# Optimization experiments

Hardware: AMD Instinct MI355X
Metric: run time of the kernel (lower is better)

The kernel has to match this reference:

```python
import jax, jax.numpy as jnp
import numpy as np

N, S, IN_F, TEXT_D, EMB, H = 128, 1024, 768, 512, 512, 8
HD = EMB // H  # 64


def setup_inputs() -> dict:
    key = jax.random.key(0)
    ks = jax.random.split(key, 14)
    sc = 0.02
    return {
        "v": jax.random.normal(ks[0], (1, N, 12, IN_F), dtype=jnp.float32),
        "t": jax.random.normal(ks[1], (N, S, TEXT_D), dtype=jnp.float32),
        "t_len": jax.random.randint(ks[2], (N,), 1, S + 1, dtype=jnp.int32),
        "W_fc1": jax.random.normal(ks[3], (EMB, IN_F), dtype=jnp.float32) * sc,
        "b_fc1": jnp.zeros((EMB,), jnp.float32),
        "W_fc2": jax.random.normal(ks[4], (EMB, 12 * EMB), dtype=jnp.float32) * sc,
        "b_fc2": jnp.zeros((EMB,), jnp.float32),
        "Wq": jax.random.normal(ks[5], (EMB, EMB), dtype=jnp.float32) * sc,
        "Wk": jax.random.normal(ks[6], (EMB, TEXT_D), dtype=jnp.float32) * sc,
        "Wv": jax.random.normal(ks[7], (EMB, TEXT_D), dtype=jnp.float32) * sc,
        "bq": jnp.zeros((EMB,), jnp.float32),
        "bk": jnp.zeros((EMB,), jnp.float32),
        "bv": jnp.zeros((EMB,), jnp.float32),
        "Wo": jax.random.normal(ks[8], (EMB, EMB), dtype=jnp.float32) * sc,
        "bo": jnp.zeros((EMB,), jnp.float32),
    }


def reference(v, t, t_len, W_fc1, b_fc1, W_fc2, b_fc2, Wq, Wk, Wv, bq, bk, bv, Wo, bo):
    # fc1 + ReLU: [1,N,12,IN_F] -> [N,12,EMB]
    x = jax.nn.relu(jnp.einsum('onif,ef->onie', v, W_fc1) + b_fc1)[0]
    # flatten + fc2 + ReLU -> [N, EMB]
    x = x.reshape(N, 12 * EMB)
    vfeat = jax.nn.relu(x @ W_fc2.T + b_fc2)
    # Batched ragged multihead attention, query length 1 per item.
    scale = 1.0 / jnp.sqrt(jnp.asarray(HD, vfeat.dtype))
    q = ((vfeat @ Wq.T + bq) * scale).reshape(N, H, HD)           # [N,H,HD]
    k = (jnp.einsum('nsd,ed->nse', t, Wk) + bk).reshape(N, S, H, HD)
    vv = (jnp.einsum('nsd,ed->nse', t, Wv) + bv).reshape(N, S, H, HD)
    scores = jnp.einsum('nhd,nshd->nhs', q, k)                    # [N,H,S]
    valid = (jnp.arange(S)[None, :] < t_len[:, None])[:, None, :]  # [N,1,S]
    scores = jnp.where(valid, scores, jnp.finfo(scores.dtype).min)
    w = jax.nn.softmax(scores, axis=-1)                           # [N,H,S]
    ctx = jnp.einsum('nhs,nshd->nhd', w, vv).reshape(N, EMB)
    attn_out = ctx @ Wo.T + bo                                    # [N,EMB]
    return vfeat, attn_out
```

## Files before the change

kernel.cpp:

```cpp
#include <hip/hip_runtime.h>

#define NB 128
#define SSEQ 1024
#define TD 512
#define TSTR 516

typedef _Float16 half8 __attribute__((ext_vector_type(8)));
typedef _Float16 half4 __attribute__((ext_vector_type(4)));
typedef float f32x4 __attribute__((ext_vector_type(4)));

template<int AM, int BM>
__device__ __forceinline__ void gemm_body(
    const void* __restrict__ Av, int lda, long aSZ,
    const void* __restrict__ Bv, int ldb, long bSZ,
    const float* __restrict__ bias, const float* __restrict__ aRowScale,
    float scale, int doRelu, int outMode,
    float* __restrict__ outF, _Float16* __restrict__ outH,
    int ldc, int cColOff, int kTiles, long oSplit,
    int mt, int nt, int sp, int bz, int tid)
{
  __shared__ _Float16 As[64][72];
  __shared__ _Float16 Bs[64][72];
  int r = tid >> 2, kq = (tid & 3) * 16;
  int w = tid >> 6, l = tid & 63;
  long aoff = (long)bz * aSZ + (long)(mt * 64 + r) * lda + (long)sp * kTiles * 64 + kq;
  long boff = (long)bz * bSZ + (long)(nt * 64 + r) * ldb + (long)sp * kTiles * 64 + kq;
  const _Float16* apH = (const _Float16*)Av + aoff;
  const float*    apF = (const float*)Av + aoff;
  const _Float16* bpH = (const _Float16*)Bv + boff;
  const float*    bpF = (const float*)Bv + boff;
  float srA = 1.0f;
  if constexpr (AM == 2) srA = 1.0f / aRowScale[(mt * 64 + r) * 8 + sp];

  half8 pa0, pa1, pb0, pb1;
  f32x4 qa0, qa1, qa2, qa3, qc0, qc1, qc2, qc3;
  if constexpr (AM == 0) { pa0 = *(const half8*)apH; pa1 = *(const half8*)(apH + 8); }
  else { qa0 = *(const f32x4*)apF; qa1 = *(const f32x4*)(apF + 4);
         qa2 = *(const f32x4*)(apF + 8); qa3 = *(const f32x4*)(apF + 12); }
  if constexpr (BM == 0) { pb0 = *(const half8*)bpH; pb1 = *(const half8*)(bpH + 8); }
  else { qc0 = *(const f32x4*)bpF; qc1 = *(const f32x4*)(bpF + 4);
         qc2 = *(const f32x4*)(bpF + 8); qc3 = *(const f32x4*)(bpF + 12); }

  f32x4 acc[4];
  #pragma unroll
  for (int c = 0; c < 4; ++c) acc[c] = (f32x4){0.f, 0.f, 0.f, 0.f};
  int fr = l & 15, fo = (l >> 4) * 8;
  for (int kt = 0; kt < kTiles; ++kt) {
    __syncthreads();
    if constexpr (AM == 0) {
      *(half8*)&As[r][kq] = pa0; *(half8*)&As[r][kq + 8] = pa1;
    } else {
      f32x4 s0 = qa0, s1 = qa1, s2 = qa2, s3 = qa3;
      if constexpr (AM == 2) { s0 *= srA; s1 *= srA; s2 *= srA; s3 *= srA; }
      *(half4*)&As[r][kq + 0]  = __builtin_convertvector(s0, half4);
      *(half4*)&As[r][kq + 4]  = __builtin_convertvector(s1, half4);
      *(half4*)&As[r][kq + 8]  = __builtin_convertvector(s2, half4);
      *(half4*)&As[r][kq + 12] = __builtin_convertvector(s3, half4);
    }
    if constexpr (BM == 0) {
      *(half8*)&Bs[r][kq] = pb0; *(half8*)&Bs[r][kq + 8] = pb1;
    } else {
      *(half4*)&Bs[r][kq + 0]  = __builtin_convertvector(qc0, half4);
      *(half4*)&Bs[r][kq + 4]  = __builtin_convertvector(qc1, half4);
      *(half4*)&Bs[r][kq + 8]  = __builtin_convertvector(qc2, half4);
      *(half4*)&Bs[r][kq + 12] = __builtin_convertvector(qc3, half4);
    }
    __syncthreads();
    if (kt + 1 < kTiles) {
      apH += 64; apF += 64; bpH += 64; bpF += 64;
      if constexpr (AM == 0) { pa0 = *(const half8*)apH; pa1 = *(const half8*)(apH + 8); }
      else { qa0 = *(const f32x4*)apF; qa1 = *(const f32x4*)(apF + 4);
             qa2 = *(const f32x4*)(apF + 8); qa3 = *(const f32x4*)(apF + 12); }
      if constexpr (BM == 0) { pb0 = *(const half8*)bpH; pb1 = *(const half8*)(bpH + 8); }
      else { qc0 = *(const f32x4*)bpF; qc1 = *(const f32x4*)(bpF + 4);
             qc2 = *(const f32x4*)(bpF + 8); qc3 = *(const f32x4*)(bpF + 12); }
    }
    #pragma unroll
    for (int ks = 0; ks < 2; ++ks) {
      half8 af = *(const half8*)&As[16 * w + fr][ks * 32 + fo];
      #pragma unroll
      for (int c = 0; c < 4; ++c) {
        half8 bf = *(const half8*)&Bs[16 * c + fr][ks * 32 + fo];
        acc[c] = __builtin_amdgcn_mfma_f32_16x16x32_f16(af, bf, acc[c], 0, 0, 0);
      }
    }
  }
  int lrow = (l >> 4) * 4, lcol = l & 15;
  #pragma unroll
  for (int c = 0; c < 4; ++c) {
    #pragma unroll
    for (int rr = 0; rr < 4; ++rr) {
      int gm = mt * 64 + 16 * w + lrow + rr;
      int gn = nt * 64 + 16 * c + lcol;
      int ecol = gn + bz * cColOff;
      float vv = acc[c][rr];
      if (bias && sp == 0) vv += bias[ecol];
      vv *= scale;
      if (doRelu) vv = fmaxf(vv, 0.f);
      long oidx = (long)gm * ldc + ecol;
      if (outMode == 0) outF[oidx] = vv;
      else if (outMode == 1) outH[oidx] = (_Float16)vv;
      else if (outMode == 2) outF[oidx + (long)sp * oSplit] = vv;
      else atomicAdd(&outF[oidx], vv);
    }
  }
}

template<int AM, int BM>
__global__ __launch_bounds__(256) void k_gemm(
    const void* __restrict__ Av, int lda, long aSZ,
    const void* __restrict__ Bv, int ldb, long bSZ,
    const float* __restrict__ bias, const float* __restrict__ aRowScale,
    float scale, int doRelu, int outMode,
    float* __restrict__ outF, _Float16* __restrict__ outH,
    int ldc, int cColOff, int mtiles, int kTiles, long oSplit)
{
  gemm_body<AM, BM>(Av, lda, aSZ, Bv, ldb, bSZ, bias, aRowScale, scale, doRelu,
                    outMode, outF, outH, ldc, cColOff, kTiles, oSplit,
                    (int)blockIdx.x % mtiles, (int)blockIdx.x / mtiles,
                    (int)blockIdx.y, (int)blockIdx.z, (int)threadIdx.x);
}

__global__ __launch_bounds__(256) void k_prepfc1(
    const float* __restrict__ Wq, const float* __restrict__ Wk,
    const float* __restrict__ bq, const float* __restrict__ bk,
    _Float16* __restrict__ G16T, float* __restrict__ gb,
    float* __restrict__ qbc, float* __restrict__ cvec,
    float* __restrict__ pz, _Float16* __restrict__ qz,
    const float* __restrict__ v, const float* __restrict__ W1,
    const float* __restrict__ b1, _Float16* __restrict__ x16,
    const float* __restrict__ Wv, const float* __restrict__ Wo,
    const float* __restrict__ bv, _Float16* __restrict__ M16,
    float* __restrict__ obo8)
{
  int bx = blockIdx.x, tid = threadIdx.x;
  if (bx >= 1024) {
    int s = bx - 1024;
    gemm_body<1, 1>(v, 768, 0, W1, 768, 0, b1, nullptr, 1.f, 1, 1,
                    nullptr, x16, 512, 0, 12, 0, s % 24, s / 24, 0, 0, tid);
    return;
  }
  __shared__ float SA[64][68];
  __shared__ float SB[64][68];
  __shared__ float sv0[64], sv1[64];
  int r = tid >> 2, cq = (tid & 3) * 16;
  int te = tid & 15, td = tid >> 4;

  if (bx >= 512) {
    int b2 = bx - 512;
    int h = b2 >> 6, et = (b2 >> 3) & 7, gt = b2 & 7;
    const float* wvp = Wv + (long)(h * 64 + r) * 512 + gt * 64 + cq;
    const float* wop = Wo + (long)(et * 64 + r) * 512 + h * 64 + cq;
    #pragma unroll
    for (int c = 0; c < 4; ++c)
      *(f32x4*)&SA[r][cq + 4 * c] = *(const f32x4*)(wvp + 4 * c);
    #pragma unroll
    for (int c = 0; c < 4; ++c) {
      f32x4 x = *(const f32x4*)(wop + 4 * c);
      #pragma unroll
      for (int i = 0; i < 4; ++i) SB[cq + 4 * c + i][r] = x[i];
    }
    if (tid < 64) sv0[tid] = bv[h * 64 + tid];
    __syncthreads();
    float acc[4][4];
    #pragma unroll
    for (int a = 0; a < 4; ++a)
      #pragma unroll
      for (int d = 0; d < 4; ++d) acc[a][d] = 0.f;
    #pragma unroll 4
    for (int jj = 0; jj < 64; ++jj) {
      f32x4 av = *(const f32x4*)&SA[jj][te * 4];
      f32x4 bt = *(const f32x4*)&SB[jj][td * 4];
      #pragma unroll
      for (int a = 0; a < 4; ++a)
        #pragma unroll
        for (int d = 0; d < 4; ++d) acc[a][d] = fmaf(av[a], bt[d], acc[a][d]);
    }
    #pragma unroll
    for (int d = 0; d < 4; ++d) {
      half4 hv = { (_Float16)acc[0][d], (_Float16)acc[1][d],
                   (_Float16)acc[2][d], (_Float16)acc[3][d] };
      *(half4*)(M16 + (long)(et * 64 + td * 4 + d) * 4096 + h * 512 + gt * 64 + te * 4) = hv;
    }
    if (gt == 0 && te == 0) {
      float s0 = 0.f, s1 = 0.f, s2 = 0.f, s3 = 0.f;
      for (int jj = 0; jj < 64; ++jj) {
        f32x4 bt = *(const f32x4*)&SB[jj][td * 4];
        float bb = sv0[jj];
        s0 = fmaf(bt[0], bb, s0); s1 = fmaf(bt[1], bb, s1);
        s2 = fmaf(bt[2], bb, s2); s3 = fmaf(bt[3], bb, s3);
      }
      obo8[h * 512 + et * 64 + td * 4 + 0] = s0;
      obo8[h * 512 + et * 64 + td * 4 + 1] = s1;
      obo8[h * 512 + et * 64 + td * 4 + 2] = s2;
      obo8[h * 512 + et * 64 + td * 4 + 3] = s3;
    }
    return;
  }

  int b = bx;
  int gid = b * 256 + tid;
  for (long i = gid; i < 131328; i += 131072)
    *(f32x4*)(pz + 4 * i) = (f32x4){0.f, 0.f, 0.f, 0.f};
  {
    long i4 = (long)gid * 4;
    long n = i4 >> 12, off = i4 & 4095;
    *(half4*)(qz + n * 8192 + 4096 + off) = (half4){(_Float16)0, (_Float16)0, (_Float16)0, (_Float16)0};
  }
  int h = b >> 6, et = (b >> 3) & 7, dt = b & 7;
  const float* wqp = Wq + (long)(h * 64 + r) * 512 + et * 64 + cq;
  const float* wkp = Wk + (long)(h * 64 + r) * 512 + dt * 64 + cq;
  #pragma unroll
  for (int c = 0; c < 4; ++c) {
    *(f32x4*)&SA[r][cq + 4 * c] = *(const f32x4*)(wqp + 4 * c);
    *(f32x4*)&SB[r][cq + 4 * c] = *(const f32x4*)(wkp + 4 * c);
  }
  if (tid < 64) { sv0[tid] = bq[h * 64 + tid]; sv1[tid] = bk[h * 64 + tid]; }
  __syncthreads();
  float acc[4][4];
  #pragma unroll
  for (int a = 0; a < 4; ++a)
    #pragma unroll
    for (int d = 0; d < 4; ++d) acc[a][d] = 0.f;
  #pragma unroll 4
  for (int j = 0; j < 64; ++j) {
    f32x4 av = *(const f32x4*)&SA[j][te * 4];
    f32x4 bv4 = *(const f32x4*)&SB[j][td * 4];
    #pragma unroll
    for (int a = 0; a < 4; ++a)
      #pragma unroll
      for (int d = 0; d < 4; ++d) acc[a][d] = fmaf(av[a], bv4[d], acc[a][d]);
  }
  #pragma unroll
  for (int d = 0; d < 4; ++d) {
    half4 hv = { (_Float16)(0.125f * acc[0][d]), (_Float16)(0.125f * acc[1][d]),
                 (_Float16)(0.125f * acc[2][d]), (_Float16)(0.125f * acc[3][d]) };
    *(half4*)(G16T + (long)h * 262144 + (long)(dt * 64 + td * 4 + d) * 512 + et * 64 + te * 4) = hv;
  }
  if (dt == 0 && td == 0) {
    #pragma unroll
    for (int i = 0; i < 4; ++i) {
      float s = 0.f;
      for (int j = 0; j < 64; ++j) s = fmaf(SA[j][te * 4 + i], sv1[j], s);
      gb[h * 512 + et * 64 + te * 4 + i] = 0.125f * s;
    }
  }
  if (et == 0 && te == 0) {
    #pragma unroll
    for (int i = 0; i < 4; ++i) {
      float s = 0.f;
      for (int j = 0; j < 64; ++j) s = fmaf(SB[j][td * 4 + i], sv0[j], s);
      cvec[h * 512 + dt * 64 + td * 4 + i] = 0.125f * s;
    }
  }
  if (et == 0 && dt == 0 && tid == 0) {
    float s = 0.f;
    for (int j = 0; j < 64; ++j) s = fmaf(sv0[j], sv1[j], s);
    qbc[h] = 0.125f * s;
  }
}

__global__ __launch_bounds__(256) void k_vfeat(
    const float* __restrict__ vacc, const float* __restrict__ b2,
    float* __restrict__ outF, _Float16* __restrict__ vf16,
    const float* __restrict__ obo8, const float* __restrict__ bo,
    float* __restrict__ obo)
{
  int i = blockIdx.x * 256 + threadIdx.x;
  float vv = b2[i & 511];
  #pragma unroll
  for (int sp = 0; sp < 16; ++sp) vv += vacc[sp * 65536 + i];
  vv = fmaxf(vv, 0.f);
  outF[i] = vv;
  vf16[i] = (_Float16)vv;
  if (i < 512) {
    float s = bo[i];
    #pragma unroll
    for (int h = 0; h < 8; ++h) s += obo8[h * 512 + i];
    obo[i] = s;
  }
}

__global__ __launch_bounds__(256) void k_qkqb(
    const _Float16* __restrict__ vf16, const _Float16* __restrict__ G16T,
    const float* __restrict__ cvec, const float* __restrict__ gb,
    const float* __restrict__ qbc, _Float16* __restrict__ qk16,
    float* __restrict__ qb, float* __restrict__ outz)
{
  int bx = blockIdx.x, tid = threadIdx.x;
  if (bx < 128) {
    int z = bx >> 4, s = bx & 15;
    gemm_body<0, 0>(vf16, 512, 0, G16T, 512, 262144, cvec, nullptr, 1.f, 0, 1,
                    nullptr, qk16, 8192, 512, 8, 0, s % 2, s / 2, 0, z, tid);
    return;
  }
  int n = bx - 128;
  float* oz = outz + (long)n * 512;
  oz[tid] = 0.f; oz[tid + 256] = 0.f;
  __shared__ float qs[512];
  qs[tid] = (float)vf16[n * 512 + tid];
  qs[tid + 256] = (float)vf16[n * 512 + tid + 256];
  __syncthreads();
  int h = tid >> 5, j = tid & 31;
  float p = 0.f;
  for (int e = j; e < 512; e += 32) p = fmaf(qs[e], gb[h * 512 + e], p);
  #pragma unroll
  for (int m = 1; m < 32; m <<= 1) p += __shfl_xor(p, m, 32);
  if (j == 0) qb[n * 8 + h] = p + qbc[h];
}

__global__ __launch_bounds__(256) void k_attn(
    const float* __restrict__ t, const int* __restrict__ tlen,
    const _Float16* __restrict__ qk16, const float* __restrict__ qb,
    float* __restrict__ pu, float* __restrict__ pl)
{
  int n = blockIdx.x >> 4, j = blockIdx.x & 15;
  int len = tlen[n];
  int base = j * 64;
  if (base >= len) return;
  int s1 = base + 64; if (s1 > len) s1 = len;
  int tid = threadIdx.x, wid = tid >> 6, l = tid & 63;
  int fr = l & 15, fo = (l >> 4) * 8;

  __shared__ __align__(16) _Float16 ts[64][TSTR];
  __shared__ __align__(16) _Float16 wst[16][72];

  const float* tn = t + (long)n * SSEQ * TD;
  {
    f32x4 a0, a1, b0, b1;
    auto ld = [&](int rr, f32x4& x0, f32x4& x1) {
      int sg = base + 16 * wid + rr;
      if (sg < s1) {
        const float* p = tn + (long)sg * TD;
        x0 = *(const f32x4*)(p + 4 * l);
        x1 = *(const f32x4*)(p + 256 + 4 * l);
      } else {
        x0 = (f32x4){0.f,0.f,0.f,0.f}; x1 = (f32x4){0.f,0.f,0.f,0.f};
      }
    };
    ld(0, a0, a1); ld(1, b0, b1);
    #pragma unroll
    for (int rr = 0; rr < 16; rr += 2) {
      half4 h0 = __builtin_convertvector(a0, half4);
      half4 h1 = __builtin_convertvector(a1, half4);
      int row = 16 * wid + rr;
      if (rr + 2 < 16) ld(rr + 2, a0, a1);
      *(half4*)&ts[row][4 * l] = h0;
      *(half4*)&ts[row][256 + 4 * l] = h1;
      half4 g0 = __builtin_convertvector(b0, half4);
      half4 g1 = __builtin_convertvector(b1, half4);
      if (rr + 3 < 16) ld(rr + 3, b0, b1);
      *(half4*)&ts[row + 1][4 * l] = g0;
      *(half4*)&ts[row + 1][256 + 4 * l] = g1;
    }
  }
  {
    const _Float16* qn = qk16 + (long)n * 8192 + fr * 512 + fo;
    float qbr = (fr < 8) ? qb[n * 8 + fr] : 0.f;
    f32x4 acc = (f32x4){0.f, 0.f, 0.f, 0.f};
    __builtin_amdgcn_s_setprio(1);
    #pragma unroll 4
    for (int kt = 0; kt < 16; ++kt) {
      half8 bf = *(const half8*)(qn + kt * 32);
      const _Float16* ap = &ts[16 * wid + fr][kt * 32 + fo];
      half4 alo = *(const half4*)ap;
      half4 ahi = *(const half4*)(ap + 4);
      half8 af = { alo[0], alo[1], alo[2], alo[3], ahi[0], ahi[1], ahi[2], ahi[3] };
      acc = __builtin_amdgcn_mfma_f32_16x16x32_f16(af, bf, acc, 0, 0, 0);
    }
    __builtin_amdgcn_s_setprio(0);
    float lac = 0.f;
    #pragma unroll
    for (int r = 0; r < 4; ++r) {
      int sl = 16 * wid + (l >> 4) * 4 + r;
      float wv = (fr < 8 && base + sl < s1) ? __expf(acc[r] + qbr) : 0.f;
      wst[fr][sl] = (_Float16)wv;
      lac += wv;
    }
    if (fr < 8) atomicAdd(&pl[n * 8 + fr], lac);
  }
  __syncthreads();
  f32x4 upv[8];
  #pragma unroll
  for (int dt = 0; dt < 8; ++dt) upv[dt] = (f32x4){0.f, 0.f, 0.f, 0.f};
  __builtin_amdgcn_s_setprio(1);
  #pragma unroll
  for (int dt = 0; dt < 8; ++dt) {
    int dcol = 128 * wid + dt * 16 + fr;
    #pragma unroll
    for (int ks = 0; ks < 2; ++ks) {
      half8 af = *(const half8*)&wst[fr][ks * 32 + fo];
      half8 bf;
      #pragma unroll
      for (int jj = 0; jj < 8; ++jj) bf[jj] = ts[ks * 32 + fo + jj][dcol];
      upv[dt] = __builtin_amdgcn_mfma_f32_16x16x32_f16(af, bf, upv[dt], 0, 0, 0);
    }
  }
  __builtin_amdgcn_s_setprio(0);
  int quad = l >> 4;
  float* pn = pu + (long)n * 4096;
  if (quad < 2) {
    #pragma unroll
    for (int dt = 0; dt < 8; ++dt) {
      int d = 128 * wid + dt * 16 + fr;
      #pragma unroll
      for (int r = 0; r < 4; ++r)
        atomicAdd(&pn[(quad * 4 + r) * 512 + d], upv[dt][r]);
    }
  }
}

extern "C" void kernel_launch(void* const* d_in, const int* in_sizes, int n_in,
                              void* d_out, int out_size, void* d_ws, size_t ws_size,
                              hipStream_t stream)
{
  const float* v    = (const float*)d_in[0];
  const float* t    = (const float*)d_in[1];
  const int*   tlen = (const int*)d_in[2];
  const float* W1   = (const float*)d_in[3];
  const float* b1   = (const float*)d_in[4];
  const float* W2   = (const float*)d_in[5];
  const float* b2   = (const float*)d_in[6];
  const float* Wq   = (const float*)d_in[7];
  const float* Wk   = (const float*)d_in[8];
  const float* Wv   = (const float*)d_in[9];
  const float* bq   = (const float*)d_in[10];
  const float* bk   = (const float*)d_in[11];
  const float* bv   = (const float*)d_in[12];
  const float* Wo   = (const float*)d_in[13];
  const float* bo   = (const float*)d_in[14];
  float* out = (float*)d_out;

  _Float16* hb   = (_Float16*)d_ws;
  _Float16* x16  = hb;
  _Float16* vf16 = hb + 786432l;
  _Float16* qk16 = hb + 851968l;
  _Float16* G16T = hb + 1900544l;
  _Float16* M16  = hb + 3997696l;
  float* fb   = (float*)(hb + 6094848l);
  float* vacc = fb;
  float* pu   = fb + 1048576l;
  float* pl   = fb + 1572864l;
  float* qb   = fb + 1573888l;
  float* gb   = fb + 1574912l;
  float* qbc  = fb + 1579008l;
  float* cvec = fb + 1579024l;
  float* obo8 = fb + 1583120l;
  float* obo  = fb + 1587216l;

  k_prepfc1<<<1216, 256, 0, stream>>>(Wq, Wk, bq, bk, G16T, gb, qbc, cvec,
                                      pu, qk16, v, W1, b1, x16, Wv, Wo, bv, M16, obo8);
  k_gemm<0,1><<<dim3(16, 16, 1), 256, 0, stream>>>(x16, 6144, 0, W2, 6144, 0,
      nullptr, nullptr, 1.f, 0, 2, vacc, nullptr, 512, 0, 2, 6, 65536);
  k_vfeat<<<256, 256, 0, stream>>>(vacc, b2, out, vf16, obo8, bo, obo);
  k_qkqb<<<256, 256, 0, stream>>>(vf16, G16T, cvec, gb, qbc, qk16, qb, out + 65536);
  k_attn<<<NB * 16, 256, 0, stream>>>(t, tlen, qk16, qb, pu, pl);
  k_gemm<2,0><<<dim3(16, 8, 1), 256, 0, stream>>>(pu, 4096, 0, M16, 4096, 0,
      obo, pl, 1.f, 0, 3, out + 65536, nullptr, 512, 0, 2, 8, 0);
}
```

Measured before the change: 476.5 us.

## Process four sequence chunks per attention block and relocate Wv·Wo fold

The attention kernel now handles 256 sequence positions per block (four 64-row chunks), accumulating the P·V partials in registers and issuing the pu/pl atomics once per block instead of once per 64-row chunk. This cuts global atomic traffic by 4x and the block count from 2048 to 512. The Wv·Wo fold moves from the prep kernel into the vfeat kernel, and the per-head bias partials obo8 are added inside the final GEMM epilogue via a new split-indexed bias, so the separate obo reduction goes away. The cost is serial chunk processing inside each block with extra barriers, and fewer blocks to hide load latency on ragged lengths.

```diff
diff --git a/kernel.cpp b/kernel.cpp
--- a/kernel.cpp
+++ b/kernel.cpp
@@ -13,7 +13,8 @@
 __device__ __forceinline__ void gemm_body(
     const void* __restrict__ Av, int lda, long aSZ,
     const void* __restrict__ Bv, int ldb, long bSZ,
-    const float* __restrict__ bias, const float* __restrict__ aRowScale,
+    const float* __restrict__ bias, const float* __restrict__ biasS,
+    const float* __restrict__ aRowScale,
     float scale, int doRelu, int outMode,
     float* __restrict__ outF, _Float16* __restrict__ outH,
     int ldc, int cColOff, int kTiles, long oSplit,
@@ -95,6 +96,7 @@
       int ecol = gn + bz * cColOff;
       float vv = acc[c][rr];
       if (bias && sp == 0) vv += bias[ecol];
+      if (biasS) vv += biasS[sp * 512 + ecol];
       vv *= scale;
       if (doRelu) vv = fmaxf(vv, 0.f);
       long oidx = (long)gm * ldc + ecol;
@@ -110,12 +112,13 @@
 __global__ __launch_bounds__(256) void k_gemm(
     const void* __restrict__ Av, int lda, long aSZ,
     const void* __restrict__ Bv, int ldb, long bSZ,
-    const float* __restrict__ bias, const float* __restrict__ aRowScale,
+    const float* __restrict__ bias, const float* __restrict__ biasS,
+    const float* __restrict__ aRowScale,
     float scale, int doRelu, int outMode,
     float* __restrict__ outF, _Float16* __restrict__ outH,
     int ldc, int cColOff, int mtiles, int kTiles, long oSplit)
 {
-  gemm_body<AM, BM>(Av, lda, aSZ, Bv, ldb, bSZ, bias, aRowScale, scale, doRelu,
+  gemm_body<AM, BM>(Av, lda, aSZ, Bv, ldb, bSZ, bias, biasS, aRowScale, scale, doRelu,
                     outMode, outF, outH, ldc, cColOff, kTiles, oSplit,
                     (int)blockIdx.x % mtiles, (int)blockIdx.x / mtiles,
                     (int)blockIdx.y, (int)blockIdx.z, (int)threadIdx.x);
@@ -128,76 +131,15 @@
     float* __restrict__ qbc, float* __restrict__ cvec,
     float* __restrict__ pz, _Float16* __restrict__ qz,
     const float* __restrict__ v, const float* __restrict__ W1,
-    const float* __restrict__ b1, _Float16* __restrict__ x16,
-    const float* __restrict__ Wv, const float* __restrict__ Wo,
-    const float* __restrict__ bv, _Float16* __restrict__ M16,
-    float* __restrict__ obo8)
+    const float* __restrict__ b1, _Float16* __restrict__ x16)
 {
   int bx = blockIdx.x, tid = threadIdx.x;
-  if (bx >= 1024) {
-    int s = bx - 1024;
-    gemm_body<1, 1>(v, 768, 0, W1, 768, 0, b1, nullptr, 1.f, 1, 1,
+  if (bx >= 512) {
+    int s = bx - 512;
+    gemm_body<1, 1>(v, 768, 0, W1, 768, 0, b1, nullptr, nullptr, 1.f, 1, 1,
                     nullptr, x16, 512, 0, 12, 0, s % 24, s / 24, 0, 0, tid);
     return;
   }
-  __shared__ float SA[64][68];
-  __shared__ float SB[64][68];
-  __shared__ float sv0[64], sv1[64];
-  int r = tid >> 2, cq = (tid & 3) * 16;
-  int te = tid & 15, td = tid >> 4;
-
-  if (bx >= 512) {
-    int b2 = bx - 512;
-    int h = b2 >> 6, et = (b2 >> 3) & 7, gt = b2 & 7;
-    const float* wvp = Wv + (long)(h * 64 + r) * 512 + gt * 64 + cq;
-    const float* wop = Wo + (long)(et * 64 + r) * 512 + h * 64 + cq;
-    #pragma unroll
-    for (int c = 0; c < 4; ++c)
-      *(f32x4*)&SA[r][cq + 4 * c] = *(const f32x4*)(wvp + 4 * c);
-    #pragma unroll
-    for (int c = 0; c < 4; ++c) {
-      f32x4 x = *(const f32x4*)(wop + 4 * c);
-      #pragma unroll
-      for (int i = 0; i < 4; ++i) SB[cq + 4 * c + i][r] = x[i];
-    }
-    if (tid < 64) sv0[tid] = bv[h * 64 + tid];
-    __syncthreads();
-    float acc[4][4];
-    #pragma unroll
-    for (int a = 0; a < 4; ++a)
-      #pragma unroll
-      for (int d = 0; d < 4; ++d) acc[a][d] = 0.f;
-    #pragma unroll 4
-    for (int jj = 0; jj < 64; ++jj) {
-      f32x4 av = *(const f32x4*)&SA[jj][te * 4];
-      f32x4 bt = *(const f32x4*)&SB[jj][td * 4];
-      #pragma unroll
-      for (int a = 0; a < 4; ++a)
-        #pragma unroll
-        for (int d = 0; d < 4; ++d) acc[a][d] = fmaf(av[a], bt[d], acc[a][d]);
-    }
-    #pragma unroll
-    for (int d = 0; d < 4; ++d) {
-      half4 hv = { (_Float16)acc[0][d], (_Float16)acc[1][d],
-                   (_Float16)acc[2][d], (_Float16)acc[3][d] };
-      *(half4*)(M16 + (long)(et * 64 + td * 4 + d) * 4096 + h * 512 + gt * 64 + te * 4) = hv;
-    }
-    if (gt == 0 && te == 0) {
-      float s0 = 0.f, s1 = 0.f, s2 = 0.f, s3 = 0.f;
-      for (int jj = 0; jj < 64; ++jj) {
-        f32x4 bt = *(const f32x4*)&SB[jj][td * 4];
-        float bb = sv0[jj];
-        s0 = fmaf(bt[0], bb, s0); s1 = fmaf(bt[1], bb, s1);
-        s2 = fmaf(bt[2], bb, s2); s3 = fmaf(bt[3], bb, s3);
-      }
-      obo8[h * 512 + et * 64 + td * 4 + 0] = s0;
-      obo8[h * 512 + et * 64 + td * 4 + 1] = s1;
-      obo8[h * 512 + et * 64 + td * 4 + 2] = s2;
-      obo8[h * 512 + et * 64 + td * 4 + 3] = s3;
-    }
-    return;
-  }
-
   int b = bx;
   int gid = b * 256 + tid;
   for (long i = gid; i < 131328; i += 131072)
@@ -207,6 +149,11 @@
     long n = i4 >> 12, off = i4 & 4095;
     *(half4*)(qz + n * 8192 + 4096 + off) = (half4){(_Float16)0, (_Float16)0, (_Float16)0, (_Float16)0};
   }
+  __shared__ float SA[64][68];
+  __shared__ float SB[64][68];
+  __shared__ float sv0[64], sv1[64];
+  int r = tid >> 2, cq = (tid & 3) * 16;
+  int te = tid & 15, td = tid >> 4;
   int h = b >> 6, et = (b >> 3) & 7, dt = b & 7;
   const float* wqp = Wq + (long)(h * 64 + r) * 512 + et * 64 + cq;
   const float* wkp = Wk + (long)(h * 64 + r) * 512 + dt * 64 + cq;
@@ -263,21 +210,73 @@
 __global__ __launch_bounds__(256) void k_vfeat(
     const float* __restrict__ vacc, const float* __restrict__ b2,
     float* __restrict__ outF, _Float16* __restrict__ vf16,
-    const float* __restrict__ obo8, const float* __restrict__ bo,
-    float* __restrict__ obo)
-{
-  int i = blockIdx.x * 256 + threadIdx.x;
-  float vv = b2[i & 511];
-  #pragma unroll
-  for (int sp = 0; sp < 16; ++sp) vv += vacc[sp * 65536 + i];
-  vv = fmaxf(vv, 0.f);
-  outF[i] = vv;
-  vf16[i] = (_Float16)vv;
-  if (i < 512) {
-    float s = bo[i];
-    #pragma unroll
-    for (int h = 0; h < 8; ++h) s += obo8[h * 512 + i];
-    obo[i] = s;
+    const float* __restrict__ Wv, const float* __restrict__ Wo,
+    const float* __restrict__ bv, _Float16* __restrict__ M16,
+    float* __restrict__ obo8)
+{
+  int bx = blockIdx.x, tid = threadIdx.x;
+  __shared__ float SA[64][68];
+  __shared__ float SB[64][68];
+  __shared__ float sv0[64];
+  if (bx < 256) {
+    int i = bx * 256 + tid;
+    float vv = b2[i & 511];
+    #pragma unroll
+    for (int sp = 0; sp < 16; ++sp) vv += vacc[sp * 65536 + i];
+    vv = fmaxf(vv, 0.f);
+    outF[i] = vv;
+    vf16[i] = (_Float16)vv;
+    return;
+  }
+  int b2i = bx - 256;
+  int h = b2i >> 6, et = (b2i >> 3) & 7, gt = b2i & 7;
+  int r = tid >> 2, cq = (tid & 3) * 16;
+  int te = tid & 15, td = tid >> 4;
+  const float* wvp = Wv + (long)(h * 64 + r) * 512 + gt * 64 + cq;
+  const float* wop = Wo + (long)(et * 64 + r) * 512 + h * 64 + cq;
+  #pragma unroll
+  for (int c = 0; c < 4; ++c)
+    *(f32x4*)&SA[r][cq + 4 * c] = *(const f32x4*)(wvp + 4 * c);
+  #pragma unroll
+  for (int c = 0; c < 4; ++c) {
+    f32x4 x = *(const f32x4*)(wop + 4 * c);
+    #pragma unroll
+    for (int i = 0; i < 4; ++i) SB[cq + 4 * c + i][r] = x[i];
+  }
+  if (tid < 64) sv0[tid] = bv[h * 64 + tid];
+  __syncthreads();
+  float acc[4][4];
+  #pragma unroll
+  for (int a = 0; a < 4; ++a)
+    #pragma unroll
+    for (int d = 0; d < 4; ++d) acc[a][d] = 0.f;
+  #pragma unroll 4
+  for (int jj = 0; jj < 64; ++jj) {
+    f32x4 av = *(const f32x4*)&SA[jj][te * 4];
+    f32x4 bt = *(const f32x4*)&SB[jj][td * 4];
+    #pragma unroll
+    for (int a = 0; a < 4; ++a)
+      #pragma unroll
+      for (int d = 0; d < 4; ++d) acc[a][d] = fmaf(av[a], bt[d], acc[a][d]);
+  }
+  #pragma unroll
+  for (int d = 0; d < 4; ++d) {
+    half4 hv = { (_Float16)acc[0][d], (_Float16)acc[1][d],
+                 (_Float16)acc[2][d], (_Float16)acc[3][d] };
+    *(half4*)(M16 + (long)(et * 64 + td * 4 + d) * 4096 + h * 512 + gt * 64 + te * 4) = hv;
+  }
+  if (gt == 0 && te == 0) {
+    float s0 = 0.f, s1 = 0.f, s2 = 0.f, s3 = 0.f;
+    for (int jj = 0; jj < 64; ++jj) {
+      f32x4 bt = *(const f32x4*)&SB[jj][td * 4];
+      float bb = sv0[jj];
+      s0 = fmaf(bt[0], bb, s0); s1 = fmaf(bt[1], bb, s1);
+      s2 = fmaf(bt[2], bb, s2); s3 = fmaf(bt[3], bb, s3);
+    }
+    obo8[h * 512 + et * 64 + td * 4 + 0] = s0;
+    obo8[h * 512 + et * 64 + td * 4 + 1] = s1;
+    obo8[h * 512 + et * 64 + td * 4 + 2] = s2;
+    obo8[h * 512 + et * 64 + td * 4 + 3] = s3;
   }
 }
 
@@ -290,7 +289,7 @@
   int bx = blockIdx.x, tid = threadIdx.x;
   if (bx < 128) {
     int z = bx >> 4, s = bx & 15;
-    gemm_body<0, 0>(vf16, 512, 0, G16T, 512, 262144, cvec, nullptr, 1.f, 0, 1,
+    gemm_body<0, 0>(vf16, 512, 0, G16T, 512, 262144, cvec, nullptr, nullptr, 1.f, 0, 1,
                     nullptr, qk16, 8192, 512, 8, 0, s % 2, s / 2, 0, z, tid);
     return;
   }
@@ -314,11 +313,9 @@
     const _Float16* __restrict__ qk16, const float* __restrict__ qb,
     float* __restrict__ pu, float* __restrict__ pl)
 {
-  int n = blockIdx.x >> 4, j = blockIdx.x & 15;
+  int n = blockIdx.x >> 2, g = blockIdx.x & 3;
   int len = tlen[n];
-  int base = j * 64;
-  if (base >= len) return;
-  int s1 = base + 64; if (s1 > len) s1 = len;
+  if (g * 256 >= len) return;
   int tid = threadIdx.x, wid = tid >> 6, l = tid & 63;
   int fr = l & 15, fo = (l >> 4) * 8;
 
@@ -326,77 +323,84 @@
   __shared__ __align__(16) _Float16 wst[16][72];
 
   const float* tn = t + (long)n * SSEQ * TD;
-  {
-    f32x4 a0, a1, b0, b1;
-    auto ld = [&](int rr, f32x4& x0, f32x4& x1) {
-      int sg = base + 16 * wid + rr;
-      if (sg < s1) {
-        const float* p = tn + (long)sg * TD;
-        x0 = *(const f32x4*)(p + 4 * l);
-        x1 = *(const f32x4*)(p + 256 + 4 * l);
-      } else {
-        x0 = (f32x4){0.f,0.f,0.f,0.f}; x1 = (f32x4){0.f,0.f,0.f,0.f};
+  const _Float16* qn = qk16 + (long)n * 8192 + fr * 512 + fo;
+  float qbr = (fr < 8) ? qb[n * 8 + fr] : 0.f;
+
+  f32x4 upv[8];
+  #pragma unroll
+  for (int dt = 0; dt < 8; ++dt) upv[dt] = (f32x4){0.f, 0.f, 0.f, 0.f};
+  float lsum = 0.f;
+
+  for (int jj = 0; jj < 4; ++jj) {
+    int base = g * 256 + jj * 64;
+    if (base >= len) break;
+    int s1 = base + 64; if (s1 > len) s1 = len;
+    if (jj) __syncthreads();
+    {
+      f32x4 a0, a1, b0, b1;
+      auto ld = [&](int rr, f32x4& x0, f32x4& x1) {
+        int sg = base + 16 * wid + rr;
+        if (sg < s1) {
+          const float* p = tn + (long)sg * TD;
+          x0 = *(const f32x4*)(p + 4 * l);
+          x1 = *(const f32x4*)(p + 256 + 4 * l);
+        } else {
+          x0 = (f32x4){0.f,0.f,0.f,0.f}; x1 = (f32x4){0.f,0.f,0.f,0.f};
+        }
+      };
+      ld(0, a0, a1); ld(1, b0, b1);
+      #pragma unroll
+      for (int rr = 0; rr < 16; rr += 2) {
+        half4 h0 = __builtin_convertvector(a0, half4);
+        half4 h1 = __builtin_convertvector(a1, half4);
+        int row = 16 * wid + rr;
+        if (rr + 2 < 16) ld(rr + 2, a0, a1);
+        *(half4*)&ts[row][4 * l] = h0;
+        *(half4*)&ts[row][256 + 4 * l] = h1;
+        half4 g0 = __builtin_convertvector(b0, half4);
+        half4 g1 = __builtin_convertvector(b1, half4);
+        if (rr + 3 < 16) ld(rr + 3, b0, b1);
+        *(half4*)&ts[row + 1][4 * l] = g0;
+        *(half4*)&ts[row + 1][256 + 4 * l] = g1;
       }
-    };
-    ld(0, a0, a1); ld(1, b0, b1);
-    #pragma unroll
-    for (int rr = 0; rr < 16; rr += 2) {
-      half4 h0 = __builtin_convertvector(a0, half4);
-      half4 h1 = __builtin_convertvector(a1, half4);
-      int row = 16 * wid + rr;
-      if (rr + 2 < 16) ld(rr + 2, a0, a1);
-      *(half4*)&ts[row][4 * l] = h0;
-      *(half4*)&ts[row][256 + 4 * l] = h1;
-      half4 g0 = __builtin_convertvector(b0, half4);
-      half4 g1 = __builtin_convertvector(b1, half4);
-      if (rr + 3 < 16) ld(rr + 3, b0, b1);
-      *(half4*)&ts[row + 1][4 * l] = g0;
-      *(half4*)&ts[row + 1][256 + 4 * l] = g1;
-    }
-  }
-  {
-    const _Float16* qn = qk16 + (long)n * 8192 + fr * 512 + fo;
-    float qbr = (fr < 8) ? qb[n * 8 + fr] : 0.f;
-    f32x4 acc = (f32x4){0.f, 0.f, 0.f, 0.f};
+    }
+    {
+      f32x4 acc = (f32x4){0.f, 0.f, 0.f, 0.f};
+      __builtin_amdgcn_s_setprio(1);
+      #pragma unroll 4
+      for (int kt = 0; kt < 16; ++kt) {
+        half8 bf = *(const half8*)(qn + kt * 32);
+        const _Float16* ap = &ts[16 * wid + fr][kt * 32 + fo];
+        half4 alo = *(const half4*)ap;
+        half4 ahi = *(const half4*)(ap + 4);
+        half8 af = { alo[0], alo[1], alo[2], alo[3], ahi[0], ahi[1], ahi[2], ahi[3] };
+        acc = __builtin_amdgcn_mfma_f32_16x16x32_f16(af, bf, acc, 0, 0, 0);
+      }
+      __builtin_amdgcn_s_setprio(0);
+      #pragma unroll
+      for (int r = 0; r < 4; ++r) {
+        int sl = 16 * wid + (l >> 4) * 4 + r;
+        float wv = (fr < 8 && base + sl < s1) ? __expf(acc[r] + qbr) : 0.f;
+        wst[fr][sl] = (_Float16)wv;
+        lsum += wv;
+      }
+    }
+    __syncthreads();
     __builtin_amdgcn_s_setprio(1);
-    #pragma unroll 4
-    for (int kt = 0; kt < 16; ++kt) {
-      half8 bf = *(const half8*)(qn + kt * 32);
-      const _Float16* ap = &ts[16 * wid + fr][kt * 32 + fo];
-      half4 alo = *(const half4*)ap;
-      half4 ahi = *(const half4*)(ap + 4);
-      half8 af = { alo[0], alo[1], alo[2], alo[3], ahi[0], ahi[1], ahi[2], ahi[3] };
-      acc = __builtin_amdgcn_mfma_f32_16x16x32_f16(af, bf, acc, 0, 0, 0);
+    #pragma unroll
+    for (int dt = 0; dt < 8; ++dt) {
+      int dcol = 128 * wid + dt * 16 + fr;
+      #pragma unroll
+      for (int ks = 0; ks < 2; ++ks) {
+        half8 af = *(const half8*)&wst[fr][ks * 32 + fo];
+        half8 bf;
+        #pragma unroll
+        for (int jx = 0; jx < 8; ++jx) bf[jx] = ts[ks * 32 + fo + jx][dcol];
+        upv[dt] = __builtin_amdgcn_mfma_f32_16x16x32_f16(af, bf, upv[dt], 0, 0, 0);
+      }
     }
     __builtin_amdgcn_s_setprio(0);
-    float lac = 0.f;
-    #pragma unroll
-    for (int r = 0; r < 4; ++r) {
-      int sl = 16 * wid + (l >> 4) * 4 + r;
-      float wv = (fr < 8 && base + sl < s1) ? __expf(acc[r] + qbr) : 0.f;
-      wst[fr][sl] = (_Float16)wv;
-      lac += wv;
-    }
-    if (fr < 8) atomicAdd(&pl[n * 8 + fr], lac);
-  }
-  __syncthreads();
-  f32x4 upv[8];
-  #pragma unroll
-  for (int dt = 0; dt < 8; ++dt) upv[dt] = (f32x4){0.f, 0.f, 0.f, 0.f};
-  __builtin_amdgcn_s_setprio(1);
-  #pragma unroll
-  for (int dt = 0; dt < 8; ++dt) {
-    int dcol = 128 * wid + dt * 16 + fr;
-    #pragma unroll
-    for (int ks = 0; ks < 2; ++ks) {
-      half8 af = *(const half8*)&wst[fr][ks * 32 + fo];
-      half8 bf;
-      #pragma unroll
-      for (int jj = 0; jj < 8; ++jj) bf[jj] = ts[ks * 32 + fo + jj][dcol];
-      upv[dt] = __builtin_amdgcn_mfma_f32_16x16x32_f16(af, bf, upv[dt], 0, 0, 0);
-    }
-  }
-  __builtin_amdgcn_s_setprio(0);
+  }
   int quad = l >> 4;
   float* pn = pu + (long)n * 4096;
   if (quad < 2) {
@@ -408,6 +412,7 @@
         atomicAdd(&pn[(quad * 4 + r) * 512 + d], upv[dt][r]);
     }
   }
+  if (fr < 8) atomicAdd(&pl[n * 8 + fr], lsum);
 }
 
 extern "C" void kernel_launch(void* const* d_in, const int* in_sizes, int n_in,
@@ -446,15 +451,14 @@
   float* qbc  = fb + 1579008l;
   float* cvec = fb + 1579024l;
   float* obo8 = fb + 1583120l;
-  float* obo  = fb + 1587216l;
-
-  k_prepfc1<<<1216, 256, 0, stream>>>(Wq, Wk, bq, bk, G16T, gb, qbc, cvec,
-                                      pu, qk16, v, W1, b1, x16, Wv, Wo, bv, M16, obo8);
+
+  k_prepfc1<<<704, 256, 0, stream>>>(Wq, Wk, bq, bk, G16T, gb, qbc, cvec,
+                                     pu, qk16, v, W1, b1, x16);
   k_gemm<0,1><<<dim3(16, 16, 1), 256, 0, stream>>>(x16, 6144, 0, W2, 6144, 0,
-      nullptr, nullptr, 1.f, 0, 2, vacc, nullptr, 512, 0, 2, 6, 65536);
-  k_vfeat<<<256, 256, 0, stream>>>(vacc, b2, out, vf16, obo8, bo, obo);
+      nullptr, nullptr, nullptr, 1.f, 0, 2, vacc, nullptr, 512, 0, 2, 6, 65536);
+  k_vfeat<<<768, 256, 0, stream>>>(vacc, b2, out, vf16, Wv, Wo, bv, M16, obo8);
   k_qkqb<<<256, 256, 0, stream>>>(vf16, G16T, cvec, gb, qbc, qk16, qb, out + 65536);
-  k_attn<<<NB * 16, 256, 0, stream>>>(t, tlen, qk16, qb, pu, pl);
+  k_attn<<<NB * 4, 256, 0, stream>>>(t, tlen, qk16, qb, pu, pl);
   k_gemm<2,0><<<dim3(16, 8, 1), 256, 0, stream>>>(pu, 4096, 0, M16, 4096, 0,
-      obo, pl, 1.f, 0, 3, out + 65536, nullptr, 512, 0, 2, 8, 0);
-}
+      bo, obo8, pl, 1.f, 0, 3, out + 65536, nullptr, 512, 0, 2, 8, 0);
+}
```

Measured after the change: 455.5 us. -4.4%, faster.
